# Performance work log

Measured on AMD Instinct MI355X. Metric: run time of the kernel, lower is better.

## Reference

```python
import jax, jax.numpy as jnp
import numpy as np

N_NODES = 50000
N_EDGES = 800000
IN_CH = 128
OUT_CH = 64
HEADS = 2
NEG_SLOPE = 0.2


def _gat_conv(x, src, dst, W, a_src, a_dst, b, n):
    """PyG-style GATConv (eval mode: no dropout), self-loops already appended.
    x: [n, F_in]; W: [F_in, H*C]; a_src/a_dst: [H, C]; b: [H*C]."""
    H, C = a_src.shape
    h = (x @ W).reshape(n, H, C)                       # [n, H, C]
    alpha_src = jnp.sum(h * a_src, axis=-1)            # [n, H]
    alpha_dst = jnp.sum(h * a_dst, axis=-1)            # [n, H]
    e = alpha_src[src] + alpha_dst[dst]                # [E, H]
    e = jnp.where(e > 0, e, NEG_SLOPE * e)             # LeakyReLU(0.2)
    # neighbor-wise (destination-grouped) softmax, numerically stable
    m = jax.ops.segment_max(e, dst, num_segments=n)
    e = jnp.exp(e - m[dst])
    denom = jax.ops.segment_sum(e, dst, num_segments=n)
    alpha = e / (denom[dst] + 1e-16)                   # [E, H]
    out = jax.ops.segment_sum(alpha[:, :, None] * h[src], dst, num_segments=n)
    return out.reshape(n, H * C) + b


def setup_inputs() -> dict:
    key = jax.random.key(0)
    ks = jax.random.split(key, 12)
    s = 0.08  # glorot-ish scale
    x = jax.random.normal(ks[0], (N_NODES, IN_CH), dtype=jnp.float32)
    edge_index = jax.random.randint(ks[1], (2, N_EDGES), 0, N_NODES, dtype=jnp.int64)
    H, O = HEADS, OUT_CH
    return {
        "x": x,
        "edge_index": edge_index,
        "W1": jax.random.normal(ks[2], (IN_CH, H * 2 * O), dtype=jnp.float32) * s,
        "a_src1": jax.random.normal(ks[3], (H, 2 * O), dtype=jnp.float32) * s,
        "a_dst1": jax.random.normal(ks[4], (H, 2 * O), dtype=jnp.float32) * s,
        "b1": jnp.zeros((H * 2 * O,), dtype=jnp.float32),
        "W_mu": jax.random.normal(ks[5], (2 * O * H, H * O), dtype=jnp.float32) * s,
        "a_src_mu": jax.random.normal(ks[6], (H, O), dtype=jnp.float32) * s,
        "a_dst_mu": jax.random.normal(ks[7], (H, O), dtype=jnp.float32) * s,
        "b_mu": jnp.zeros((H * O,), dtype=jnp.float32),
        "W_ls": jax.random.normal(ks[8], (2 * O * H, H * O), dtype=jnp.float32) * s,
        "a_src_ls": jax.random.normal(ks[9], (H, O), dtype=jnp.float32) * s,
        "a_dst_ls": jax.random.normal(ks[10], (H, O), dtype=jnp.float32) * s,
        "b_ls": jnp.zeros((H * O,), dtype=jnp.float32),
    }


def reference(x, edge_index, W1, a_src1, a_dst1, b1,
              W_mu, a_src_mu, a_dst_mu, b_mu,
              W_ls, a_src_ls, a_dst_ls, b_ls):
    n = x.shape[0]
    loop = jnp.arange(n, dtype=edge_index.dtype)
    src = jnp.concatenate([edge_index[0], loop])  # PyG add_self_loops=True
    dst = jnp.concatenate([edge_index[1], loop])
    x1 = jax.nn.elu(_gat_conv(x, src, dst, W1, a_src1, a_dst1, b1, n))
    mu = _gat_conv(x1, src, dst, W_mu, a_src_mu, a_dst_mu, b_mu, n)
    logstd = _gat_conv(x1, src, dst, W_ls, a_src_ls, a_dst_ls, b_ls, n)
    return (mu, logstd)
```

## Files before the change

kernel.cpp:

```cpp
#include <hip/hip_runtime.h>


typedef unsigned short u16;
typedef unsigned int u32;
typedef _Float16 f16;
typedef f16 f16x8 __attribute__((ext_vector_type(8)));
typedef float f32x4v __attribute__((ext_vector_type(4)));

__device__ __forceinline__ u16 f2h(float f) {
    union { f16 h; u16 u; } t;
    t.h = (f16)f;
    return t.u;
}
__device__ __forceinline__ float4 loadh4(const u16* __restrict__ p, size_t i) {
    union { uint2 u; f16 h[4]; } t;
    t.u = *(const uint2*)(p + i);
    return make_float4((float)t.h[0], (float)t.h[1], (float)t.h[2], (float)t.h[3]);
}
__device__ __forceinline__ void store4(float* __restrict__ p, size_t i, float4 v) {
    *(float4*)(p + i) = v;
}
__device__ __forceinline__ void store4(u16* __restrict__ p, size_t i, float4 v) {
    union { uint2 u; f16 h[4]; } t;
    t.h[0] = (f16)v.x; t.h[1] = (f16)v.y; t.h[2] = (f16)v.z; t.h[3] = (f16)v.w;
    *(uint2*)(p + i) = t.u;
}

__global__ __launch_bounds__(256) void k_detect(const u32* __restrict__ ebuf,
                                                int* __restrict__ flag) {
    __shared__ int nz;
    if (threadIdx.x == 0) nz = 0;
    __syncthreads();
    if (ebuf[2 * threadIdx.x + 1] != 0u) atomicAdd(&nz, 1);
    __syncthreads();
    if (threadIdx.x == 0) *flag = (nz == 0) ? 1 : 0;
}

__global__ __launch_bounds__(256) void k_extract(const u32* __restrict__ ebuf, int E,
                                                 const int* __restrict__ flag,
                                                 int* __restrict__ se,
                                                 int* __restrict__ de,
                                                 int* __restrict__ deg) {
    int e = blockIdx.x * 256 + threadIdx.x;
    if (e >= E) return;
    int s, d;
    if (*flag) {
        s = (int)ebuf[2 * (size_t)e];
        d = (int)ebuf[2 * ((size_t)E + (size_t)e)];
    } else {
        s = (int)ebuf[e];
        d = (int)ebuf[(size_t)E + (size_t)e];
    }
    se[e] = s;
    de[e] = d;
    atomicAdd(&deg[d], 1);
}

__global__ __launch_bounds__(256) void k_scan_a(const int* __restrict__ deg, int n,
                                                int* __restrict__ bsum) {
    __shared__ int s[256];
    int i = blockIdx.x * 256 + threadIdx.x;
    s[threadIdx.x] = (i < n) ? deg[i] : 0;
    __syncthreads();
    for (int st = 128; st > 0; st >>= 1) {
        if (threadIdx.x < st) s[threadIdx.x] += s[threadIdx.x + st];
        __syncthreads();
    }
    if (threadIdx.x == 0) bsum[blockIdx.x] = s[0];
}

__global__ __launch_bounds__(256) void k_scan_b(int* __restrict__ bsum, int nb) {
    __shared__ int s[256];
    int t = threadIdx.x;
    int v = (t < nb) ? bsum[t] : 0;
    s[t] = v;
    __syncthreads();
    for (int off = 1; off < 256; off <<= 1) {
        int add = (t >= off) ? s[t - off] : 0;
        __syncthreads();
        s[t] += add;
        __syncthreads();
    }
    if (t < nb) bsum[t] = s[t] - v;
}

__global__ __launch_bounds__(256) void k_scan_c(const int* __restrict__ deg, int n,
                                                const int* __restrict__ bsum,
                                                int* __restrict__ rowptr,
                                                int* __restrict__ cursor, int E) {
    __shared__ int s[256];
    int t = threadIdx.x;
    int i = blockIdx.x * 256 + t;
    int v = (i < n) ? deg[i] : 0;
    s[t] = v;
    __syncthreads();
    for (int off = 1; off < 256; off <<= 1) {
        int add = (t >= off) ? s[t - off] : 0;
        __syncthreads();
        s[t] += add;
        __syncthreads();
    }
    if (i < n) {
        int ex = bsum[blockIdx.x] + s[t] - v;
        rowptr[i] = ex;
        cursor[i] = ex;
    }
    if (i == 0) rowptr[n] = E;
}

__global__ __launch_bounds__(256) void k_fill(const int* __restrict__ src,
                                              const int* __restrict__ dst, int E,
                                              int* __restrict__ cursor,
                                              int* __restrict__ csr_src,
                                              int* __restrict__ csr_dst) {
    int e = blockIdx.x * 256 + threadIdx.x;
    if (e < E) {
        int d = dst[e];
        int slot = atomicAdd(&cursor[d], 1);
        csr_src[slot] = src[e];
        csr_dst[slot] = d;
    }
}

__global__ __launch_bounds__(256) void k_cvt(const float* __restrict__ in,
                                             u16* __restrict__ out, int nElem) {
    int i = (blockIdx.x * 256 + threadIdx.x) * 4;
    if (i >= nElem) return;
    float4 v = *(const float4*)(in + i);
    store4(out, i, v);
}

__global__ __launch_bounds__(256) void k_tw(const float* __restrict__ Wl,
                                            const float* __restrict__ Wr, int split,
                                            int K, u16* __restrict__ Wt) {
    int idx = blockIdx.x * 256 + threadIdx.x;
    if (idx >= 256 * K) return;
    int c = idx / K, k = idx - c * K;
    float v;
    if (split == 256)
        v = Wl[(size_t)k * 256 + c];
    else
        v = (c < 128) ? Wl[(size_t)k * 128 + c] : Wr[(size_t)k * 128 + (c - 128)];
    Wt[idx] = f2h(v);
}

template <int NS>
__global__ __launch_bounds__(256) void k_w(const int* __restrict__ csr_src,
                                           const int* __restrict__ csr_dst,
                                           const float* __restrict__ as,
                                           const float* __restrict__ ad,
                                           float* __restrict__ wp, int E) {
    int i = blockIdx.x * 256 + threadIdx.x;
    if (i >= E) return;
    int s = csr_src[i], d = csr_dst[i];
    if (NS == 2) {
        float2 a = *(const float2*)(as + (size_t)s * 2);
        float2 b = *(const float2*)(ad + (size_t)d * 2);
        float e0 = a.x + b.x, e1 = a.y + b.y;
        e0 = fmaxf(e0, 0.2f * e0);
        e1 = fmaxf(e1, 0.2f * e1);
        wp[i] = __expf(e0);
        wp[(size_t)E + i] = __expf(e1);
    } else {
        float4 a = *(const float4*)(as + (size_t)s * 4);
        float4 b = *(const float4*)(ad + (size_t)d * 4);
        float e0 = a.x + b.x, e1 = a.y + b.y, e2 = a.z + b.z, e3 = a.w + b.w;
        e0 = fmaxf(e0, 0.2f * e0);
        e1 = fmaxf(e1, 0.2f * e1);
        e2 = fmaxf(e2, 0.2f * e2);
        e3 = fmaxf(e3, 0.2f * e3);
        wp[i] = __expf(e0);
        wp[(size_t)E + i] = __expf(e1);
        wp[2 * (size_t)E + i] = __expf(e2);
        wp[3 * (size_t)E + i] = __expf(e3);
    }
}

template <int K, int ALOGW>
__global__ __launch_bounds__(256) void k_gemm_mfma(
    const u16* __restrict__ Ah, const u16* __restrict__ Wt, u16* __restrict__ out,
    float* __restrict__ as_out, float* __restrict__ ad_out,
    const float* __restrict__ alo, const float* __restrict__ ahi,
    const float* __restrict__ dlo, const float* __restrict__ dhi, int M) {
    __shared__ u16 Bs[256 * 40];
    const int tid = threadIdx.x;
    const int wave = tid >> 6;
    const int lane = tid & 63;
    const int li = lane & 15;
    const int quad = lane >> 4;
    const int r0 = blockIdx.x * 64 + wave * 16;
    int arowi = r0 + li;
    if (arowi >= M) arowi = M - 1;
    const u16* arow = Ah + (size_t)arowi * K + quad * 8;

    f32x4v acc[16];
#pragma unroll
    for (int ct = 0; ct < 16; ct++) acc[ct] = (f32x4v)(0.f);

    for (int t = 0; t < K; t += 32) {
        __syncthreads();
        {
            const u16* src = Wt + (size_t)tid * K + t;
            u16* dst = Bs + tid * 40;
            uint4 v0 = ((const uint4*)src)[0];
            uint4 v1 = ((const uint4*)src)[1];
            uint4 v2 = ((const uint4*)src)[2];
            uint4 v3 = ((const uint4*)src)[3];
            ((uint4*)dst)[0] = v0;
            ((uint4*)(dst + 8))[0] = v1;
            ((uint4*)(dst + 16))[0] = v2;
            ((uint4*)(dst + 24))[0] = v3;
        }
        __syncthreads();
        f16x8 a = *(const f16x8*)(arow + t);
#pragma unroll
        for (int ct = 0; ct < 16; ct++) {
            f16x8 b = *(const f16x8*)(Bs + (ct * 16 + li) * 40 + quad * 8);
            acc[ct] = __builtin_amdgcn_mfma_f32_16x16x32_f16(a, b, acc[ct], 0, 0, 0);
        }
    }

#pragma unroll
    for (int reg = 0; reg < 4; reg++) {
        int grow = r0 + quad * 4 + reg;
        if (grow < M) {
            u16* orow = out + (size_t)grow * 256 + li;
#pragma unroll
            for (int ct = 0; ct < 16; ct++) orow[ct * 16] = f2h(acc[ct][reg]);
        }
    }

    const int NS = 64 >> ALOGW;
    const int SH = ALOGW - 2;
    float aw[16], dw[16];
#pragma unroll
    for (int ct = 0; ct < 16; ct++) {
        int col = ct * 16 + li;
        aw[ct] = (col < 128) ? alo[col] : ahi[col - 128];
        dw[ct] = (col < 128) ? dlo[col] : dhi[col - 128];
    }
#pragma unroll
    for (int reg = 0; reg < 4; reg++) {
        float s[4] = {0.f, 0.f, 0.f, 0.f};
        float d[4] = {0.f, 0.f, 0.f, 0.f};
#pragma unroll
        for (int ct = 0; ct < 16; ct++) {
            int sl = ct >> SH;
            s[sl] += acc[ct][reg] * aw[ct];
            d[sl] += acc[ct][reg] * dw[ct];
        }
#pragma unroll
        for (int sl = 0; sl < NS; sl++) {
#pragma unroll
            for (int m = 1; m <= 8; m <<= 1) {
                s[sl] += __shfl_xor(s[sl], m, 64);
                d[sl] += __shfl_xor(d[sl], m, 64);
            }
        }
        int grow = r0 + quad * 4 + reg;
        if (li == 0 && grow < M) {
#pragma unroll
            for (int sl = 0; sl < NS; sl++) {
                as_out[(size_t)grow * NS + sl] = s[sl];
                ad_out[(size_t)grow * NS + sl] = d[sl];
            }
        }
    }
}

template <int LOGW, int MODE, typename OT>
__global__ __launch_bounds__(256) void k_agg4(
    const u16* __restrict__ h, const int* __restrict__ rowptr,
    const int* __restrict__ csr_src, const float* __restrict__ wp,
    const float* __restrict__ as, const float* __restrict__ ad,
    const float* __restrict__ b_lo, const float* __restrict__ b_hi,
    OT* __restrict__ outp, int n, int nGrp, int E) {
    const int NS = 64 >> LOGW;
    const int bid = blockIdx.x;
    const int xcd = bid & 7;
    const int half = xcd >> 2;
    const int grp = (bid >> 3) * 4 + (xcd & 3);
    if (grp >= nGrp) return;
    const int lane = threadIdx.x & 63;
    const int sub = lane >> 5;
    const int sl = lane & 31;
    const int wid0 = grp * 8 + (threadIdx.x >> 6) * 2 + sub;
    const bool ok = wid0 < n;
    const int wid = ok ? wid0 : (n - 1);
    const int col = half * 128 + sl * 4;
    const int slot = col >> (LOGW + 2);
    const float* __restrict__ wpl = wp + (size_t)slot * E;

    float e = as[(size_t)wid * NS + slot] + ad[(size_t)wid * NS + slot];
    e = fmaxf(e, 0.2f * e);
    float w = __expf(e);
    float denom = w;
    float4 hv = loadh4(h, (size_t)wid * 256 + col);
    float acc0 = w * hv.x, acc1 = w * hv.y, acc2 = w * hv.z, acc3 = w * hv.w;

    int rb = 0, re = 0;
    if (ok) { rb = rowptr[wid0]; re = rowptr[wid0 + 1]; }
    int p = rb;
    for (; p + 8 <= re; p += 8) {
        int4 sA = *(const int4*)(csr_src + p);
        int4 sB = *(const int4*)(csr_src + p + 4);
        float4 wA = *(const float4*)(wpl + p);
        float4 wB = *(const float4*)(wpl + p + 4);
        float4 h0 = loadh4(h, (size_t)sA.x * 256 + col);
        float4 h1 = loadh4(h, (size_t)sA.y * 256 + col);
        float4 h2 = loadh4(h, (size_t)sA.z * 256 + col);
        float4 h3 = loadh4(h, (size_t)sA.w * 256 + col);
        float4 h4 = loadh4(h, (size_t)sB.x * 256 + col);
        float4 h5 = loadh4(h, (size_t)sB.y * 256 + col);
        float4 h6 = loadh4(h, (size_t)sB.z * 256 + col);
        float4 h7 = loadh4(h, (size_t)sB.w * 256 + col);
        denom += (wA.x + wA.y + wA.z + wA.w) + (wB.x + wB.y + wB.z + wB.w);
        acc0 += wA.x * h0.x + wA.y * h1.x + wA.z * h2.x + wA.w * h3.x +
                wB.x * h4.x + wB.y * h5.x + wB.z * h6.x + wB.w * h7.x;
        acc1 += wA.x * h0.y + wA.y * h1.y + wA.z * h2.y + wA.w * h3.y +
                wB.x * h4.y + wB.y * h5.y + wB.z * h6.y + wB.w * h7.y;
        acc2 += wA.x * h0.z + wA.y * h1.z + wA.z * h2.z + wA.w * h3.z +
                wB.x * h4.z + wB.y * h5.z + wB.z * h6.z + wB.w * h7.z;
        acc3 += wA.x * h0.w + wA.y * h1.w + wA.z * h2.w + wA.w * h3.w +
                wB.x * h4.w + wB.y * h5.w + wB.z * h6.w + wB.w * h7.w;
    }
    for (; p + 4 <= re; p += 4) {
        int4 sA = *(const int4*)(csr_src + p);
        float4 wA = *(const float4*)(wpl + p);
        float4 h0 = loadh4(h, (size_t)sA.x * 256 + col);
        float4 h1 = loadh4(h, (size_t)sA.y * 256 + col);
        float4 h2 = loadh4(h, (size_t)sA.z * 256 + col);
        float4 h3 = loadh4(h, (size_t)sA.w * 256 + col);
        denom += (wA.x + wA.y) + (wA.z + wA.w);
        acc0 += wA.x * h0.x + wA.y * h1.x + wA.z * h2.x + wA.w * h3.x;
        acc1 += wA.x * h0.y + wA.y * h1.y + wA.z * h2.y + wA.w * h3.y;
        acc2 += wA.x * h0.z + wA.y * h1.z + wA.z * h2.z + wA.w * h3.z;
        acc3 += wA.x * h0.w + wA.y * h1.w + wA.z * h2.w + wA.w * h3.w;
    }
    for (; p < re; ++p) {
        int s = csr_src[p];
        float ww = wpl[p];
        float4 hh = loadh4(h, (size_t)s * 256 + col);
        denom += ww;
        acc0 += ww * hh.x;
        acc1 += ww * hh.y;
        acc2 += ww * hh.z;
        acc3 += ww * hh.w;
    }
    float inv = 1.0f / (denom + 1e-16f);

    const float* bp = half ? b_hi : b_lo;
    const int ci = sl * 4;
    float4 bv = *(const float4*)(bp + ci);
    float v0 = acc0 * inv + bv.x;
    float v1 = acc1 * inv + bv.y;
    float v2 = acc2 * inv + bv.z;
    float v3 = acc3 * inv + bv.w;

    if (!ok) return;
    if (MODE == 0) {
        v0 = v0 > 0.f ? v0 : expm1f(v0);
        v1 = v1 > 0.f ? v1 : expm1f(v1);
        v2 = v2 > 0.f ? v2 : expm1f(v2);
        v3 = v3 > 0.f ? v3 : expm1f(v3);
        store4((u16*)outp, (size_t)wid0 * 256 + col, make_float4(v0, v1, v2, v3));
    } else {
        size_t base = half ? ((size_t)n * 128 + (size_t)wid0 * 128 + ci)
                           : ((size_t)wid0 * 128 + ci);
        store4((float*)outp, base, make_float4(v0, v1, v2, v3));
    }
}

extern "C" void kernel_launch(void* const* d_in, const int* in_sizes, int n_in,
                              void* d_out, int out_size, void* d_ws, size_t ws_size,
                              hipStream_t stream) {
    const float* x = (const float*)d_in[0];
    const u32* ebuf = (const u32*)d_in[1];
    const float* W1 = (const float*)d_in[2];
    const float* a_src1 = (const float*)d_in[3];
    const float* a_dst1 = (const float*)d_in[4];
    const float* b1 = (const float*)d_in[5];
    const float* W_mu = (const float*)d_in[6];
    const float* a_src_mu = (const float*)d_in[7];
    const float* a_dst_mu = (const float*)d_in[8];
    const float* b_mu = (const float*)d_in[9];
    const float* W_ls = (const float*)d_in[10];
    const float* a_src_ls = (const float*)d_in[11];
    const float* a_dst_ls = (const float*)d_in[12];
    const float* b_ls = (const float*)d_in[13];

    const int n = in_sizes[0] / 128;
    const int E = in_sizes[1] / 2;

    char* base = (char*)d_ws;
    size_t off = 0;
    auto alloc = [&](size_t b) -> char* {
        char* p = base + off;
        off = (off + b + 255) & ~(size_t)255;
        return p;
    };
    int* rowptr = (int*)alloc((size_t)(n + 1) * 4);
    int* cursor = (int*)alloc((size_t)n * 4);
    int* csr = (int*)alloc((size_t)E * 4);
    int* csrd = (int*)alloc((size_t)E * 4);
    int* bsum = (int*)alloc(256 * 4);
    int* eflag = (int*)alloc(256);
    int* se = (int*)alloc((size_t)E * 4);
    int* de = (int*)alloc((size_t)E * 4);
    float* as = (float*)alloc((size_t)n * 4 * 4);
    float* ad = (float*)alloc((size_t)n * 4 * 4);
    float* wp = (float*)alloc((size_t)E * 4 * 4);
    u16* W1t = (u16*)alloc(256 * 128 * 2);
    u16* Wt2 = (u16*)alloc(256 * 256 * 2);
    u16* x1h = (u16*)alloc((size_t)n * 256 * 2);
    u16* xh = x1h;
    u16* h = (u16*)alloc((size_t)n * 256 * 2);

    const int nb = (n + 255) / 256;
    const int eg = (E + 255) / 256;
    const int gg = (n + 63) / 64;
    const int nGrp = (n + 7) / 8;
    const int aggGrid = 8 * ((nGrp + 3) / 4);

    hipMemsetAsync(cursor, 0, (size_t)n * 4, stream);
    k_detect<<<1, 256, 0, stream>>>(ebuf, eflag);
    k_extract<<<eg, 256, 0, stream>>>(ebuf, E, eflag, se, de, cursor);
    k_scan_a<<<nb, 256, 0, stream>>>(cursor, n, bsum);
    k_scan_b<<<1, 256, 0, stream>>>(bsum, nb);
    k_scan_c<<<nb, 256, 0, stream>>>(cursor, n, bsum, rowptr, cursor, E);
    k_fill<<<eg, 256, 0, stream>>>(se, de, E, cursor, csr, csrd);

    k_cvt<<<(n * 128 / 4 + 255) / 256, 256, 0, stream>>>(x, xh, n * 128);
    k_tw<<<(256 * 128 + 255) / 256, 256, 0, stream>>>(W1, W1, 256, 128, W1t);
    k_tw<<<(256 * 256 + 255) / 256, 256, 0, stream>>>(W_mu, W_ls, 128, 256, Wt2);

    k_gemm_mfma<128, 5><<<gg, 256, 0, stream>>>(xh, W1t, h, as, ad, a_src1,
                                                a_src1 + 128, a_dst1, a_dst1 + 128,
                                                n);
    k_w<2><<<eg, 256, 0, stream>>>(csr, csrd, as, ad, wp, E);
    k_agg4<5, 0, u16><<<aggGrid, 256, 0, stream>>>(h, rowptr, csr, wp, as, ad, b1,
                                                   b1 + 128, x1h, n, nGrp, E);

    k_gemm_mfma<256, 4><<<gg, 256, 0, stream>>>(x1h, Wt2, h, as, ad, a_src_mu,
                                                a_src_ls, a_dst_mu, a_dst_ls, n);
    k_w<4><<<eg, 256, 0, stream>>>(csr, csrd, as, ad, wp, E);
    k_agg4<4, 1, float><<<aggGrid, 256, 0, stream>>>(h, rowptr, csr, wp, as, ad,
                                                     b_mu, b_ls, (float*)d_out, n,
                                                     nGrp, E);
}
```

Baseline: 391.8 us.

## Fuse fp32-to-fp16 input conversion into GEMM, double rows per wave, prefetch tiles

The separate x conversion kernel is removed, and the first GEMM now reads fp32 x directly and converts it to fp16 in registers. Each wave now computes 32 rows instead of 16, so every B tile loaded into LDS feeds twice as many MFMAs and the grid is halved. The next W and A tiles are also prefetched into registers during the current iteration, with raw barriers replacing __syncthreads. This removes one kernel launch and a round trip of x through memory, in exchange for more registers per thread (two accumulator sets) and lower occupancy.

```diff
diff --git a/kernel.cpp b/kernel.cpp
--- a/kernel.cpp
+++ b/kernel.cpp
@@ -120,14 +120,6 @@
         csr_src[slot] = src[e];
         csr_dst[slot] = d;
     }
-}
-
-__global__ __launch_bounds__(256) void k_cvt(const float* __restrict__ in,
-                                             u16* __restrict__ out, int nElem) {
-    int i = (blockIdx.x * 256 + threadIdx.x) * 4;
-    if (i >= nElem) return;
-    float4 v = *(const float4*)(in + i);
-    store4(out, i, v);
 }
 
 __global__ __launch_bounds__(256) void k_tw(const float* __restrict__ Wl,
@@ -176,9 +168,9 @@
     }
 }
 
-template <int K, int ALOGW>
+template <int K, int ALOGW, bool AF32>
 __global__ __launch_bounds__(256) void k_gemm_mfma(
-    const u16* __restrict__ Ah, const u16* __restrict__ Wt, u16* __restrict__ out,
+    const void* __restrict__ Av, const u16* __restrict__ Wt, u16* __restrict__ out,
     float* __restrict__ as_out, float* __restrict__ ad_out,
     const float* __restrict__ alo, const float* __restrict__ ahi,
     const float* __restrict__ dlo, const float* __restrict__ dhi, int M) {
@@ -188,45 +180,90 @@
     const int lane = tid & 63;
     const int li = lane & 15;
     const int quad = lane >> 4;
-    const int r0 = blockIdx.x * 64 + wave * 16;
-    int arowi = r0 + li;
-    if (arowi >= M) arowi = M - 1;
-    const u16* arow = Ah + (size_t)arowi * K + quad * 8;
-
-    f32x4v acc[16];
-#pragma unroll
-    for (int ct = 0; ct < 16; ct++) acc[ct] = (f32x4v)(0.f);
+    const int r0 = blockIdx.x * 128 + wave * 32;
+    int ar0 = r0 + li;
+    int ar1 = r0 + 16 + li;
+    if (ar0 >= M) ar0 = M - 1;
+    if (ar1 >= M) ar1 = M - 1;
+    const u16* a16_0 = (const u16*)Av + (size_t)ar0 * K + quad * 8;
+    const u16* a16_1 = (const u16*)Av + (size_t)ar1 * K + quad * 8;
+    const float* a32_0 = (const float*)Av + (size_t)ar0 * K + quad * 8;
+    const float* a32_1 = (const float*)Av + (size_t)ar1 * K + quad * 8;
+
+    f32x4v acc0[16], acc1[16];
+#pragma unroll
+    for (int ct = 0; ct < 16; ct++) {
+        acc0[ct] = (f32x4v)(0.f);
+        acc1[ct] = (f32x4v)(0.f);
+    }
+
+    const u16* wrow = Wt + (size_t)tid * K;
+    u16* dstp = Bs + tid * 40;
+    uint4 sv0 = ((const uint4*)wrow)[0];
+    uint4 sv1 = ((const uint4*)(wrow + 8))[0];
+    uint4 sv2 = ((const uint4*)(wrow + 16))[0];
+    uint4 sv3 = ((const uint4*)(wrow + 24))[0];
+    uint4 p0a, p0b, p1a, p1b;
+    if (AF32) {
+        p0a = *(const uint4*)(a32_0);
+        p0b = *(const uint4*)(a32_0 + 4);
+        p1a = *(const uint4*)(a32_1);
+        p1b = *(const uint4*)(a32_1 + 4);
+    } else {
+        p0a = *(const uint4*)(a16_0);
+        p1a = *(const uint4*)(a16_1);
+        p0b = p0a;
+        p1b = p1a;
+    }
 
     for (int t = 0; t < K; t += 32) {
-        __syncthreads();
-        {
-            const u16* src = Wt + (size_t)tid * K + t;
-            u16* dst = Bs + tid * 40;
-            uint4 v0 = ((const uint4*)src)[0];
-            uint4 v1 = ((const uint4*)src)[1];
-            uint4 v2 = ((const uint4*)src)[2];
-            uint4 v3 = ((const uint4*)src)[3];
-            ((uint4*)dst)[0] = v0;
-            ((uint4*)(dst + 8))[0] = v1;
-            ((uint4*)(dst + 16))[0] = v2;
-            ((uint4*)(dst + 24))[0] = v3;
+        asm volatile("s_waitcnt lgkmcnt(0)" ::: "memory");
+        __builtin_amdgcn_s_barrier();
+        ((uint4*)dstp)[0] = sv0;
+        ((uint4*)(dstp + 8))[0] = sv1;
+        ((uint4*)(dstp + 16))[0] = sv2;
+        ((uint4*)(dstp + 24))[0] = sv3;
+        f16x8 a0, a1;
+        if (AF32) {
+            union { uint4 u; float f[4]; } ua, ub;
+            ua.u = p0a; ub.u = p0b;
+            a0[0] = (f16)ua.f[0]; a0[1] = (f16)ua.f[1];
+            a0[2] = (f16)ua.f[2]; a0[3] = (f16)ua.f[3];
+            a0[4] = (f16)ub.f[0]; a0[5] = (f16)ub.f[1];
+            a0[6] = (f16)ub.f[2]; a0[7] = (f16)ub.f[3];
+            ua.u = p1a; ub.u = p1b;
+            a1[0] = (f16)ua.f[0]; a1[1] = (f16)ua.f[1];
+            a1[2] = (f16)ua.f[2]; a1[3] = (f16)ua.f[3];
+            a1[4] = (f16)ub.f[0]; a1[5] = (f16)ub.f[1];
+            a1[6] = (f16)ub.f[2]; a1[7] = (f16)ub.f[3];
+        } else {
+            union { uint4 u; f16x8 h; } uh;
+            uh.u = p0a; a0 = uh.h;
+            uh.u = p1a; a1 = uh.h;
         }
-        __syncthreads();
-        f16x8 a = *(const f16x8*)(arow + t);
+        if (t + 32 < K) {
+            const u16* s2 = wrow + t + 32;
+            sv0 = ((const uint4*)s2)[0];
+            sv1 = ((const uint4*)(s2 + 8))[0];
+            sv2 = ((const uint4*)(s2 + 16))[0];
+            sv3 = ((const uint4*)(s2 + 24))[0];
+            if (AF32) {
+                p0a = *(const uint4*)(a32_0 + t + 32);
+                p0b = *(const uint4*)(a32_0 + t + 36);
+                p1a = *(const uint4*)(a32_1 + t + 32);
+                p1b = *(const uint4*)(a32_1 + t + 36);
+            } else {
+                p0a = *(const uint4*)(a16_0 + t + 32);
+                p1a = *(const uint4*)(a16_1 + t + 32);
+            }
+        }
+        asm volatile("s_waitcnt lgkmcnt(0)" ::: "memory");
+        __builtin_amdgcn_s_barrier();
 #pragma unroll
         for (int ct = 0; ct < 16; ct++) {
             f16x8 b = *(const f16x8*)(Bs + (ct * 16 + li) * 40 + quad * 8);
-            acc[ct] = __builtin_amdgcn_mfma_f32_16x16x32_f16(a, b, acc[ct], 0, 0, 0);
-        }
-    }
-
-#pragma unroll
-    for (int reg = 0; reg < 4; reg++) {
-        int grow = r0 + quad * 4 + reg;
-        if (grow < M) {
-            u16* orow = out + (size_t)grow * 256 + li;
-#pragma unroll
-            for (int ct = 0; ct < 16; ct++) orow[ct * 16] = f2h(acc[ct][reg]);
+            acc0[ct] = __builtin_amdgcn_mfma_f32_16x16x32_f16(a0, b, acc0[ct], 0, 0, 0);
+            acc1[ct] = __builtin_amdgcn_mfma_f32_16x16x32_f16(a1, b, acc1[ct], 0, 0, 0);
         }
     }
 
@@ -239,33 +276,47 @@
         aw[ct] = (col < 128) ? alo[col] : ahi[col - 128];
         dw[ct] = (col < 128) ? dlo[col] : dhi[col - 128];
     }
-#pragma unroll
-    for (int reg = 0; reg < 4; reg++) {
-        float s[4] = {0.f, 0.f, 0.f, 0.f};
-        float d[4] = {0.f, 0.f, 0.f, 0.f};
-#pragma unroll
-        for (int ct = 0; ct < 16; ct++) {
-            int sl = ct >> SH;
-            s[sl] += acc[ct][reg] * aw[ct];
-            d[sl] += acc[ct][reg] * dw[ct];
-        }
-#pragma unroll
-        for (int sl = 0; sl < NS; sl++) {
-#pragma unroll
-            for (int m = 1; m <= 8; m <<= 1) {
-                s[sl] += __shfl_xor(s[sl], m, 64);
-                d[sl] += __shfl_xor(d[sl], m, 64);
+
+    auto epilogue = [&](f32x4v(&acc)[16], int rbase) {
+#pragma unroll
+        for (int reg = 0; reg < 4; reg++) {
+            int grow = rbase + quad * 4 + reg;
+            if (grow < M) {
+                u16* orow = out + (size_t)grow * 256 + li;
+#pragma unroll
+                for (int ct = 0; ct < 16; ct++) orow[ct * 16] = f2h(acc[ct][reg]);
             }
         }
-        int grow = r0 + quad * 4 + reg;
-        if (li == 0 && grow < M) {
+#pragma unroll
+        for (int reg = 0; reg < 4; reg++) {
+            float s[4] = {0.f, 0.f, 0.f, 0.f};
+            float d[4] = {0.f, 0.f, 0.f, 0.f};
+#pragma unroll
+            for (int ct = 0; ct < 16; ct++) {
+                int sl = ct >> SH;
+                s[sl] += acc[ct][reg] * aw[ct];
+                d[sl] += acc[ct][reg] * dw[ct];
+            }
 #pragma unroll
             for (int sl = 0; sl < NS; sl++) {
-                as_out[(size_t)grow * NS + sl] = s[sl];
-                ad_out[(size_t)grow * NS + sl] = d[sl];
+#pragma unroll
+                for (int m = 1; m <= 8; m <<= 1) {
+                    s[sl] += __shfl_xor(s[sl], m, 64);
+                    d[sl] += __shfl_xor(d[sl], m, 64);
+                }
+            }
+            int grow = rbase + quad * 4 + reg;
+            if (li == 0 && grow < M) {
+#pragma unroll
+                for (int sl = 0; sl < NS; sl++) {
+                    as_out[(size_t)grow * NS + sl] = s[sl];
+                    ad_out[(size_t)grow * NS + sl] = d[sl];
+                }
             }
         }
-    }
+    };
+    epilogue(acc0, r0);
+    epilogue(acc1, r0 + 16);
 }
 
 template <int LOGW, int MODE, typename OT>
@@ -413,12 +464,11 @@
     u16* W1t = (u16*)alloc(256 * 128 * 2);
     u16* Wt2 = (u16*)alloc(256 * 256 * 2);
     u16* x1h = (u16*)alloc((size_t)n * 256 * 2);
-    u16* xh = x1h;
     u16* h = (u16*)alloc((size_t)n * 256 * 2);
 
     const int nb = (n + 255) / 256;
     const int eg = (E + 255) / 256;
-    const int gg = (n + 63) / 64;
+    const int gg = (n + 127) / 128;
     const int nGrp = (n + 7) / 8;
     const int aggGrid = 8 * ((nGrp + 3) / 4);
 
@@ -430,19 +480,19 @@
     k_scan_c<<<nb, 256, 0, stream>>>(cursor, n, bsum, rowptr, cursor, E);
     k_fill<<<eg, 256, 0, stream>>>(se, de, E, cursor, csr, csrd);
 
-    k_cvt<<<(n * 128 / 4 + 255) / 256, 256, 0, stream>>>(x, xh, n * 128);
     k_tw<<<(256 * 128 + 255) / 256, 256, 0, stream>>>(W1, W1, 256, 128, W1t);
     k_tw<<<(256 * 256 + 255) / 256, 256, 0, stream>>>(W_mu, W_ls, 128, 256, Wt2);
 
-    k_gemm_mfma<128, 5><<<gg, 256, 0, stream>>>(xh, W1t, h, as, ad, a_src1,
-                                                a_src1 + 128, a_dst1, a_dst1 + 128,
-                                                n);
+    k_gemm_mfma<128, 5, true><<<gg, 256, 0, stream>>>(x, W1t, h, as, ad, a_src1,
+                                                      a_src1 + 128, a_dst1,
+                                                      a_dst1 + 128, n);
     k_w<2><<<eg, 256, 0, stream>>>(csr, csrd, as, ad, wp, E);
     k_agg4<5, 0, u16><<<aggGrid, 256, 0, stream>>>(h, rowptr, csr, wp, as, ad, b1,
                                                    b1 + 128, x1h, n, nGrp, E);
 
-    k_gemm_mfma<256, 4><<<gg, 256, 0, stream>>>(x1h, Wt2, h, as, ad, a_src_mu,
-                                                a_src_ls, a_dst_mu, a_dst_ls, n);
+    k_gemm_mfma<256, 4, false><<<gg, 256, 0, stream>>>(x1h, Wt2, h, as, ad,
+                                                       a_src_mu, a_src_ls,
+                                                       a_dst_mu, a_dst_ls, n);
     k_w<4><<<eg, 256, 0, stream>>>(csr, csrd, as, ad, wp, E);
     k_agg4<4, 1, float><<<aggGrid, 256, 0, stream>>>(h, rowptr, csr, wp, as, ad,
                                                      b_mu, b_ls, (float*)d_out, n,
```

Result: no change. 388.4 us (-0.9%).
